# Kernel optimization log

Hardware: AMD Instinct MI355X
Metric: run time of the kernel (lower is better)

## Reference

```python
import jax, jax.numpy as jnp
import numpy as np
from jax import lax

B, S, PH, N = 4, 512, 4096, 16384
D, G, H, L, FF, GS = 1024, 128, 8, 4, 4096, 32
HD = D // H


def setup_inputs() -> dict:
    key = jax.random.key(0)
    ks = list(jax.random.split(key, 16))
    r = lambda k, sh: jax.random.normal(k, sh, jnp.float32) * 0.02
    return {
        'last_hidden': jax.random.normal(ks[0], (B, S, PH), jnp.float32),
        'current_pointcloud': jax.random.normal(ks[1], (B, N, 3), jnp.float32),
        'fp_w': r(ks[2], (D, PH)), 'fp_b': jnp.zeros((D,), jnp.float32),
        'sp_w': r(ks[3], (G * D, D)), 'sp_b': jnp.zeros((G * D,), jnp.float32),
        'pos_embed': r(ks[4], (1, G, D)),
        'ln1_w': jnp.ones((L, D), jnp.float32), 'ln1_b': jnp.zeros((L, D), jnp.float32),
        'in_w': r(ks[5], (L, 3 * D, D)), 'in_b': jnp.zeros((L, 3 * D), jnp.float32),
        'out_w': r(ks[6], (L, D, D)), 'out_b': jnp.zeros((L, D), jnp.float32),
        'ln2_w': jnp.ones((L, D), jnp.float32), 'ln2_b': jnp.zeros((L, D), jnp.float32),
        'mlp_w1': r(ks[7], (L, FF, D)), 'mlp_b1': jnp.zeros((L, FF), jnp.float32),
        'mlp_w2': r(ks[8], (L, D, FF)), 'mlp_b2': jnp.zeros((L, D), jnp.float32),
        'c1_w': r(ks[9], (D, D)), 'c1_b': jnp.zeros((D,), jnp.float32),
        'bn_g': jnp.ones((D,), jnp.float32), 'bn_beta': jnp.zeros((D,), jnp.float32),
        'bn_m': jnp.zeros((D,), jnp.float32), 'bn_v': jnp.ones((D,), jnp.float32),
        'c2_w': r(ks[10], (3 * GS, D)), 'c2_b': jnp.zeros((3 * GS,), jnp.float32),
    }


def _ln(x, w, b):
    m = jnp.mean(x, -1, keepdims=True)
    v = jnp.mean(jnp.square(x - m), -1, keepdims=True)
    return (x - m) * lax.rsqrt(v + 1e-5) * w + b


def _fps(xyz, num_samples):
    # iterative farthest point sampling; deterministic start index 0
    Bb, Nn, _ = xyz.shape
    dist0 = jnp.full((Bb, Nn), 1e10, xyz.dtype)
    far0 = jnp.zeros((Bb,), jnp.int32)

    def step(carry, _):
        dist, far = carry
        centroid = jnp.take_along_axis(xyz, far[:, None, None], axis=1)  # [B,1,3]
        d = jnp.sum(jnp.square(xyz - centroid), -1)                      # [B,N]
        dist = jnp.minimum(dist, d)
        return (dist, jnp.argmax(dist, -1).astype(jnp.int32)), far

    _, cents = lax.scan(step, (dist0, far0), None, length=num_samples)
    cents = cents.T  # [B, num_samples]
    return jnp.take_along_axis(xyz, cents[:, :, None], axis=1)  # [B,num_samples,3]


def reference(last_hidden, current_pointcloud, fp_w, fp_b, sp_w, sp_b, pos_embed,
              ln1_w, ln1_b, in_w, in_b, out_w, out_b, ln2_w, ln2_b,
              mlp_w1, mlp_b1, mlp_w2, mlp_b2,
              c1_w, c1_b, bn_g, bn_beta, bn_m, bn_v, c2_w, c2_b):
    bsz = last_hidden.shape[0]
    agg = jnp.mean(last_hidden @ fp_w.T + fp_b, axis=1)          # [B,D]
    x = (agg @ sp_w.T + sp_b).reshape(bsz, G, D)                 # [B,G,D]
    centers = _fps(current_pointcloud, G)                        # [B,G,3]
    scale = 1.0 / np.sqrt(HD).astype(np.float32)

    def block(x, p):
        l1w, l1b, iw, ib, ow, ob, l2w, l2b, w1, b1, w2, b2 = p
        xn = _ln(x + pos_embed, l1w, l1b)
        qkv = xn @ iw.T + ib                                     # [B,G,3D]
        q, k, v = jnp.split(qkv, 3, axis=-1)
        hsp = lambda t: t.reshape(bsz, G, H, HD).transpose(0, 2, 1, 3)
        q, k, v = hsp(q), hsp(k), hsp(v)
        a = jax.nn.softmax(jnp.einsum('bhqd,bhkd->bhqk', q, k) * scale, axis=-1)
        o = jnp.einsum('bhqk,bhkd->bhqd', a, v).transpose(0, 2, 1, 3).reshape(bsz, G, D)
        x = x + o @ ow.T + ob
        h = jax.nn.gelu(_ln(x, l2w, l2b) @ w1.T + b1, approximate=False)
        return x + h @ w2.T + b2, None

    x, _ = lax.scan(block, x, (ln1_w, ln1_b, in_w, in_b, out_w, out_b,
                               ln2_w, ln2_b, mlp_w1, mlp_b1, mlp_w2, mlp_b2))

    # future_predictor: 1x1 conv == per-token linear; BN in eval mode
    h = x @ c1_w.T + c1_b
    h = jax.nn.relu((h - bn_m) * lax.rsqrt(bn_v + 1e-5) * bn_g + bn_beta)
    deltas = (h @ c2_w.T + c2_b).reshape(bsz * G, GS, 3)
    pred = deltas + centers.reshape(bsz * G, 1, 3)
    return pred.reshape(bsz, G * GS, 3)
```

## Files before the change

### kernel.cpp

```cpp
#include <hip/hip_runtime.h>
#include <hip/hip_bf16.h>
#include <math.h>


typedef __bf16 bf16x8_t __attribute__((ext_vector_type(8)));
typedef float  f32x4_t  __attribute__((ext_vector_type(4)));

__device__ __forceinline__ float wredsum(float v){
#pragma unroll
  for (int o = 32; o; o >>= 1) v += __shfl_down(v, o, 64);
  return v;
}

__device__ __forceinline__ bf16x8_t pack8(float4 a, float4 b){
  bf16x8_t v;
  v[0]=(__bf16)a.x; v[1]=(__bf16)a.y; v[2]=(__bf16)a.z; v[3]=(__bf16)a.w;
  v[4]=(__bf16)b.x; v[5]=(__bf16)b.y; v[6]=(__bf16)b.z; v[7]=(__bf16)b.w;
  return v;
}

__device__ __forceinline__ void gload16(const void* g, void* l){
  __builtin_amdgcn_global_load_lds((const __attribute__((address_space(1))) unsigned int*)g,
                                   (__attribute__((address_space(3))) unsigned int*)l, 16, 0, 0);
}

__global__ __launch_bounds__(1024) void fused_front(
  const float* __restrict__ pc, float* __restrict__ centers,
  const float* __restrict__ agg, const float* __restrict__ spw,
  const float* __restrict__ spb, float* __restrict__ x,
  const float* __restrict__ inw, const float* __restrict__ outw,
  const float* __restrict__ w1, const float* __restrict__ w2,
  const float* __restrict__ c1w, __bf16* __restrict__ wbf)
{
  const int bid = blockIdx.x;
  const int tid = threadIdx.x;
  if (bid < 4){
    const int b = bid;
    const int lane = tid & 63;
    const float* base = pc + (size_t)b * 16384 * 3;
    float px[16], py[16], pz[16], dist[16];
    {
      union { float4 v4[12]; float f[48]; } u;
      const float4* src = (const float4*)(base + tid * 48);
#pragma unroll
      for (int q = 0; q < 12; ++q) u.v4[q] = src[q];
#pragma unroll
      for (int j = 0; j < 16; ++j){
        px[j] = u.f[j*3]; py[j] = u.f[j*3+1]; pz[j] = u.f[j*3+2];
        dist[j] = 1e10f;
      }
    }
    __shared__ unsigned long long keyslot[128];
    for (int i = tid; i < 128; i += 1024) keyslot[i] = 0ULL;
    __syncthreads();
    float cx = base[0], cy = base[1], cz = base[2];
    for (int t = 0; t < 128; ++t){
      if (tid == 0){
        centers[(b*128+t)*3+0] = cx;
        centers[(b*128+t)*3+1] = cy;
        centers[(b*128+t)*3+2] = cz;
      }
      if (t == 127) break;
      float bmax = -1.0f; int bidx = 0;
#pragma unroll
      for (int j = 0; j < 16; ++j){
        float dx = __fsub_rn(px[j], cx);
        float dy = __fsub_rn(py[j], cy);
        float dz = __fsub_rn(pz[j], cz);
        float d  = __fadd_rn(__fadd_rn(__fmul_rn(dx,dx), __fmul_rn(dy,dy)), __fmul_rn(dz,dz));
        float nd = fminf(dist[j], d);
        dist[j] = nd;
        if (nd > bmax){ bmax = nd; bidx = tid*16 + j; }
      }
      unsigned long long key = ((unsigned long long)__float_as_uint(bmax) << 32)
                             | (unsigned long long)(0xFFFFFFFFu - (unsigned)bidx);
#pragma unroll
      for (int o = 32; o; o >>= 1){
        unsigned long long ok = __shfl_down(key, o, 64);
        if (ok > key) key = ok;
      }
      if (lane == 0) atomicMax(&keyslot[t], key);
      __syncthreads();
      const unsigned long long gk = keyslot[t];
      const unsigned gidx = 0xFFFFFFFFu - (unsigned)(gk & 0xFFFFFFFFu);
      const float* cp = base + (size_t)gidx*3;
      cx = cp[0]; cy = cp[1]; cz = cp[2];
    }
  } else if (bid < 1028){
    __shared__ float ag[4096];
    for (int i = tid; i < 4096; i += 1024) ag[i] = agg[i];
    __syncthreads();
    const int wv = tid >> 6, lane = tid & 63;
    const int rbase = ((bid - 4)*16 + wv)*8;
    for (int rr = 0; rr < 8; ++rr){
      const int row = rbase + rr;
      const float* wp = spw + (size_t)row*1024 + lane*4;
      const float4 w0 = *(const float4*)(wp      );
      const float4 wq1 = *(const float4*)(wp + 256);
      const float4 wq2 = *(const float4*)(wp + 512);
      const float4 wq3 = *(const float4*)(wp + 768);
      float acc[4];
#pragma unroll
      for (int bb = 0; bb < 4; ++bb){
        const float* gp = &ag[bb*1024 + lane*4];
        const float4 g0 = *(const float4*)(gp      );
        const float4 g1 = *(const float4*)(gp + 256);
        const float4 g2 = *(const float4*)(gp + 512);
        const float4 g3 = *(const float4*)(gp + 768);
        acc[bb] = w0.x*g0.x + w0.y*g0.y + w0.z*g0.z + w0.w*g0.w
                + wq1.x*g1.x + wq1.y*g1.y + wq1.z*g1.z + wq1.w*g1.w
                + wq2.x*g2.x + wq2.y*g2.y + wq2.z*g2.z + wq2.w*g2.w
                + wq3.x*g3.x + wq3.y*g3.y + wq3.z*g3.z + wq3.w*g3.w;
      }
      float a0 = wredsum(acc[0]);
      float a1 = wredsum(acc[1]);
      float a2 = wredsum(acc[2]);
      float a3 = wredsum(acc[3]);
      if (lane == 0){
        const float bias = spb[row];
        x[(size_t)0*131072 + row] = a0 + bias;
        x[(size_t)1*131072 + row] = a1 + bias;
        x[(size_t)2*131072 + row] = a2 + bias;
        x[(size_t)3*131072 + row] = a3 + bias;
      }
    }
  } else {
    const size_t t = (size_t)(bid - 1028)*1024 + tid;
    const size_t i = t*8;
    const float* src;
    if (i < 50331648){
      const size_t l = i / 12582912, r = i - l*12582912;
      if (r < 3145728)       src = inw  + l*3145728 + r;
      else if (r < 4194304)  src = outw + l*1048576 + (r-3145728);
      else if (r < 8388608)  src = w1   + l*4194304 + (r-4194304);
      else                   src = w2   + l*4194304 + (r-8388608);
    } else src = c1w + (i - 50331648);
    float4 a = *(const float4*)src, bq = *(const float4*)(src+4);
    *(bf16x8_t*)(wbf + i) = pack8(a, bq);
  }
}

__global__ __launch_bounds__(256) void partial_kernel(const float* __restrict__ lh,
                                                      float* __restrict__ part){
  const int ph = blockIdx.x*256 + threadIdx.x;
  const int sc = blockIdx.y, b = blockIdx.z;
  const float* p = lh + ((size_t)b*512 + sc*64)*4096 + ph;
  float s0=0,s1=0,s2=0,s3=0;
  for (int j = 0; j < 64; j += 4){
    s0 += p[(size_t)(j+0)*4096];
    s1 += p[(size_t)(j+1)*4096];
    s2 += p[(size_t)(j+2)*4096];
    s3 += p[(size_t)(j+3)*4096];
  }
  part[(size_t)(b*8+sc)*4096 + ph] = (s0+s1)+(s2+s3);
}

__global__ __launch_bounds__(256) void combine_kernel(const float* __restrict__ part,
                                                      float* __restrict__ mlh){
  const int i = blockIdx.x*256 + threadIdx.x;
  const int b = i >> 12, ph = i & 4095;
  float s = 0;
#pragma unroll
  for (int sc = 0; sc < 8; ++sc) s += part[(size_t)(b*8+sc)*4096 + ph];
  mlh[i] = s * (1.0f/512.0f);
}

__global__ __launch_bounds__(256) void agg_kernel(const float* __restrict__ mlh,
                                                  const float* __restrict__ fpw,
                                                  const float* __restrict__ fpb,
                                                  float* __restrict__ agg){
  const int o = blockIdx.x*4 + (threadIdx.x>>6);
  const int lane = threadIdx.x & 63;
  const int b = o >> 10, d = o & 1023;
  const float* mp = mlh + b*4096;
  const float* wp = fpw + (size_t)d*4096;
  float s = 0;
#pragma unroll 4
  for (int j = 0; j < 64; ++j){
    int ph = lane + j*64;
    s += mp[ph] * wp[ph];
  }
  s = wredsum(s);
  if (lane == 0) agg[o] = s + fpb[d];
}

__global__ __launch_bounds__(256) void ln_kernel(const float* __restrict__ x,
                                                 const float* __restrict__ pos,
                                                 const float* __restrict__ w,
                                                 const float* __restrict__ bb,
                                                 __bf16* __restrict__ out){
  const int tok = blockIdx.x, g = tok & 127, t = threadIdx.x;
  const int lane = t & 63, wv = t >> 6;
  const float* xr = x + (size_t)tok*1024;
  float v[4];
#pragma unroll
  for (int j = 0; j < 4; ++j){
    int d = t + j*256;
    float val = xr[d];
    if (pos) val += pos[g*1024 + d];
    v[j] = val;
  }
  __shared__ float r1[4], r2[4];
  float s = wredsum(v[0]+v[1]+v[2]+v[3]);
  if (lane == 0) r1[wv] = s;
  __syncthreads();
  const float mean = (r1[0]+r1[1]+r1[2]+r1[3]) * (1.0f/1024.0f);
  float sq = 0;
#pragma unroll
  for (int j = 0; j < 4; ++j){ float d0 = v[j]-mean; sq += d0*d0; }
  sq = wredsum(sq);
  if (lane == 0) r2[wv] = sq;
  __syncthreads();
  const float var = (r2[0]+r2[1]+r2[2]+r2[3]) * (1.0f/1024.0f);
  const float rs = rsqrtf(var + 1e-5f);
#pragma unroll
  for (int j = 0; j < 4; ++j){
    int d = t + j*256;
    out[(size_t)tok*1024 + d] = (__bf16)((v[j]-mean)*rs*w[d] + bb[d]);
  }
}

__global__ __launch_bounds__(256) void gemm_sk(
  const __bf16* __restrict__ A, const __bf16* __restrict__ W,
  float* __restrict__ parts, int M, int N, int K, int kc)
{
  __shared__ __bf16 As[4][128*32];
  __shared__ __bf16 Ws[4][128*32];
  const int n0 = blockIdx.x*128, m0 = blockIdx.y*128, z = blockIdx.z;
  const int tid = threadIdx.x;
  const int lane = tid & 63, w = tid >> 6;
  const int wm = w >> 1, wn = w & 1;
  const int lr = lane & 15, g = lane >> 4;
  const int kbeg = z*kc;
  const int nst = kc >> 5;
  const int c0 = tid, c1 = tid + 256;
  const int r0 = c0 >> 2, q0 = c0 & 3;
  const int r1 = c1 >> 2, q1 = c1 & 3;
  const __bf16* a0 = A + (size_t)(m0 + r0)*K + kbeg + q0*8;
  const __bf16* a1 = A + (size_t)(m0 + r1)*K + kbeg + q1*8;
  const __bf16* w0 = W + (size_t)(n0 + r0)*K + kbeg + q0*8;
  const __bf16* w1 = W + (size_t)(n0 + r1)*K + kbeg + q1*8;

#define STAGE(BUF, KOFF) do { \
    gload16(a0 + (KOFF), &As[(BUF)][c0*8]); \
    gload16(a1 + (KOFF), &As[(BUF)][c1*8]); \
    gload16(w0 + (KOFF), &Ws[(BUF)][c0*8]); \
    gload16(w1 + (KOFF), &Ws[(BUF)][c1*8]); \
  } while(0)

  STAGE(0, 0);
  STAGE(1, 32);
  STAGE(2, 64);
  f32x4_t acc[4][4] = {};
  for (int t = 0; t < nst; ++t){
    asm volatile("s_waitcnt vmcnt(8)" ::: "memory");
    __builtin_amdgcn_s_barrier();
    const int tnext = (t+3 < nst) ? (t+3) : (nst-1);
    STAGE((t+3)&3, tnext*32);
    const int cb = t & 3;
    bf16x8_t af[4], bf[4];
#pragma unroll
    for (int f = 0; f < 4; ++f){
      af[f] = *(bf16x8_t*)&As[cb][(wm*64 + f*16 + lr)*32 + g*8];
      bf[f] = *(bf16x8_t*)&Ws[cb][(wn*64 + f*16 + lr)*32 + g*8];
    }
#pragma unroll
    for (int i = 0; i < 4; ++i)
#pragma unroll
      for (int j = 0; j < 4; ++j)
        acc[i][j] = __builtin_amdgcn_mfma_f32_16x16x32_bf16(af[i], bf[j], acc[i][j], 0, 0, 0);
  }
#undef STAGE
  float* C = parts + (size_t)z*M*N;
#pragma unroll
  for (int i = 0; i < 4; ++i)
#pragma unroll
    for (int j = 0; j < 4; ++j)
#pragma unroll
      for (int r = 0; r < 4; ++r){
        const int row = m0 + wm*64 + i*16 + g*4 + r;
        const int col = n0 + wn*64 + j*16 + lr;
        C[(size_t)row*N + col] = acc[i][j][r];
      }
}

__global__ __launch_bounds__(256) void comb_qkv(const float* __restrict__ parts,
                                                const float* __restrict__ bias,
                                                __bf16* __restrict__ out){
  const int i = blockIdx.x*256 + threadIdx.x;
  const int col = i % 3072;
  out[i] = (__bf16)(parts[i] + parts[1572864 + i] + bias[col]);
}

__global__ __launch_bounds__(256) void comb_gelu(const float* __restrict__ parts,
                                                 const float* __restrict__ bias,
                                                 __bf16* __restrict__ out){
  const int i = blockIdx.x*256 + threadIdx.x;
  const int col = i & 4095;
  float v = parts[i] + parts[2097152 + i] + bias[col];
  v = v * 0.5f * (1.0f + erff(v * 0.70710678118654752440f));
  out[i] = (__bf16)v;
}

template<int MODE>
__global__ __launch_bounds__(256) void comb_res_ln(const float* __restrict__ parts, int nsplit,
                                                   const float* __restrict__ bias,
                                                   const float* __restrict__ pos,
                                                   const float* __restrict__ lw,
                                                   const float* __restrict__ lb,
                                                   float* __restrict__ x,
                                                   __bf16* __restrict__ xn){
  const int tok = blockIdx.x, gi = tok & 127, t = threadIdx.x;
  const int lane = t & 63, wv = t >> 6;
  float v[4];
#pragma unroll
  for (int j = 0; j < 4; ++j){
    const int d = t + j*256;
    const size_t idx = (size_t)tok*1024 + d;
    float s = 0;
    for (int z = 0; z < nsplit; ++z) s += parts[(size_t)z*524288 + idx];
    float val = x[idx] + s + bias[d];
    x[idx] = val;
    v[j] = val;
  }
  if (MODE == 2){
#pragma unroll
    for (int j = 0; j < 4; ++j){
      const int d = t + j*256;
      xn[(size_t)tok*1024 + d] = (__bf16)v[j];
    }
    return;
  }
  float u[4];
#pragma unroll
  for (int j = 0; j < 4; ++j){
    const int d = t + j*256;
    u[j] = v[j] + (MODE == 1 ? pos[gi*1024 + d] : 0.0f);
  }
  __shared__ float r1[4], r2[4];
  float s1 = wredsum(u[0]+u[1]+u[2]+u[3]);
  if (lane == 0) r1[wv] = s1;
  __syncthreads();
  const float mean = (r1[0]+r1[1]+r1[2]+r1[3]) * (1.0f/1024.0f);
  float sq = 0;
#pragma unroll
  for (int j = 0; j < 4; ++j){ float d0 = u[j]-mean; sq += d0*d0; }
  sq = wredsum(sq);
  if (lane == 0) r2[wv] = sq;
  __syncthreads();
  const float var = (r2[0]+r2[1]+r2[2]+r2[3]) * (1.0f/1024.0f);
  const float rs = rsqrtf(var + 1e-5f);
#pragma unroll
  for (int j = 0; j < 4; ++j){
    const int d = t + j*256;
    xn[(size_t)tok*1024 + d] = (__bf16)((u[j]-mean)*rs*lw[d] + lb[d]);
  }
}

__global__ __launch_bounds__(256) void attn_fused(const __bf16* __restrict__ qkv,
                                                  __bf16* __restrict__ O){
  const int bh = blockIdx.x >> 1, half = blockIdx.x & 1;
  const int b = bh>>3, h = bh&7;
  const int tid = threadIdx.x, w = tid>>6, lane = tid&63;
  const int lr = lane&15, g = lane>>4;
  __shared__ __bf16 vt[128*128];
  __shared__ __bf16 pl[4*2048];
  {
    const int n = tid >> 1, kh = tid & 1;
    const __bf16* vbase = qkv + (size_t)(b*128)*3072 + 2048 + h*128 + n;
#pragma unroll
    for (int jb = 0; jb < 8; ++jb){
      bf16x8_t pk;
#pragma unroll
      for (int e = 0; e < 8; ++e) pk[e] = vbase[(size_t)(kh*64 + jb*8 + e)*3072];
      const int cb = kh*8 + jb;
      *(bf16x8_t*)&vt[n*128 + ((cb ^ (n&7)) * 8)] = pk;
    }
  }
  const __bf16* qbase = qkv + (size_t)(b*128)*3072 + h*128;
  const __bf16* kbase = qbase + 1024;
  const int qrow0 = half*64 + w*16;
  f32x4_t acc[8] = {};
#pragma unroll
  for (int ks = 0; ks < 4; ++ks){
    bf16x8_t aq, bk[8];
    aq = *(const bf16x8_t*)(qbase + (size_t)(qrow0 + lr)*3072 + ks*32 + g*8);
#pragma unroll
    for (int j = 0; j < 8; ++j)
      bk[j] = *(const bf16x8_t*)(kbase + (size_t)(j*16 + lr)*3072 + ks*32 + g*8);
#pragma unroll
    for (int j = 0; j < 8; ++j)
      acc[j] = __builtin_amdgcn_mfma_f32_16x16x32_bf16(aq, bk[j], acc[j], 0, 0, 0);
  }
  __syncthreads();
  const float scale = 0.088388347648318447f;
#pragma unroll
  for (int r = 0; r < 4; ++r){
    const int row = g*4 + r;
    float sv[8];
    float mx = -1e30f;
#pragma unroll
    for (int j = 0; j < 8; ++j){ sv[j] = acc[j][r]*scale; mx = fmaxf(mx, sv[j]); }
#pragma unroll
    for (int o = 1; o < 16; o <<= 1) mx = fmaxf(mx, __shfl_xor(mx, o, 64));
    float s = 0;
#pragma unroll
    for (int j = 0; j < 8; ++j){ sv[j] = expf(sv[j]-mx); s += sv[j]; }
#pragma unroll
    for (int o = 1; o < 16; o <<= 1) s += __shfl_xor(s, o, 64);
    const float inv = 1.0f/s;
#pragma unroll
    for (int j = 0; j < 8; ++j){
      const int col = j*16 + lr;
      const int slot = (col>>3) ^ (row&7);
      pl[w*2048 + row*128 + slot*8 + (lr&7)] = (__bf16)(sv[j]*inv);
    }
  }
  __syncthreads();
  f32x4_t acc2[8] = {};
#pragma unroll
  for (int ks = 0; ks < 4; ++ks){
    bf16x8_t ap, bv[8];
    {
      const int row = lr;
      const int slot = (ks*4 + g) ^ (row&7);
      ap = *(bf16x8_t*)&pl[w*2048 + row*128 + slot*8];
    }
#pragma unroll
    for (int j = 0; j < 8; ++j){
      const int rowv = j*16 + lr;
      const int cb = ks*4 + g;
      bv[j] = *(bf16x8_t*)&vt[rowv*128 + ((cb ^ (rowv&7))*8)];
    }
#pragma unroll
    for (int j = 0; j < 8; ++j)
      acc2[j] = __builtin_amdgcn_mfma_f32_16x16x32_bf16(ap, bv[j], acc2[j], 0, 0, 0);
  }
#pragma unroll
  for (int j = 0; j < 8; ++j)
#pragma unroll
    for (int r = 0; r < 4; ++r){
      const int row = qrow0 + g*4 + r;
      const int col = j*16 + lr;
      O[(size_t)(b*128+row)*1024 + h*128 + col] = (__bf16)acc2[j][r];
    }
}

__global__ __launch_bounds__(256) void head_kernel(const float* __restrict__ parts,
                                                   const float* __restrict__ c1b,
                                                   const float* __restrict__ bnm,
                                                   const float* __restrict__ bnv,
                                                   const float* __restrict__ bng,
                                                   const float* __restrict__ bnb,
                                                   const float* __restrict__ c2w,
                                                   const float* __restrict__ c2b,
                                                   const float* __restrict__ centers,
                                                   float* __restrict__ out){
  const int tok = blockIdx.x, t = threadIdx.x;
  const int wv = t >> 6, lane = t & 63;
  __shared__ float hrow[1024];
#pragma unroll
  for (int j = 0; j < 4; ++j){
    const int d = t + j*256;
    const size_t idx = (size_t)tok*1024 + d;
    float s = 0;
#pragma unroll
    for (int z = 0; z < 8; ++z) s += parts[(size_t)z*524288 + idx];
    float v = s + c1b[d];
    v = (v - bnm[d]) * rsqrtf(bnv[d] + 1e-5f) * bng[d] + bnb[d];
    hrow[d] = fmaxf(v, 0.0f);
  }
  __syncthreads();
  for (int i = 0; i < 24; ++i){
    const int n = wv*24 + i;
    const float* wp = c2w + (size_t)n*1024;
    float s = 0;
#pragma unroll 4
    for (int j = 0; j < 16; ++j){
      const int k = lane + j*64;
      s += hrow[k] * wp[k];
    }
    s = wredsum(s);
    if (lane == 0) out[(size_t)tok*96 + n] = s + c2b[n] + centers[tok*3 + (n % 3)];
  }
}

extern "C" void kernel_launch(void* const* d_in, const int* in_sizes, int n_in,
                              void* d_out, int out_size, void* d_ws, size_t ws_size,
                              hipStream_t stream){
  const float* lh   = (const float*)d_in[0];
  const float* pc   = (const float*)d_in[1];
  const float* fpw  = (const float*)d_in[2];
  const float* fpb  = (const float*)d_in[3];
  const float* spw  = (const float*)d_in[4];
  const float* spb  = (const float*)d_in[5];
  const float* pos  = (const float*)d_in[6];
  const float* ln1w = (const float*)d_in[7];
  const float* ln1b = (const float*)d_in[8];
  const float* inw  = (const float*)d_in[9];
  const float* inb  = (const float*)d_in[10];
  const float* outw = (const float*)d_in[11];
  const float* outb = (const float*)d_in[12];
  const float* ln2w = (const float*)d_in[13];
  const float* ln2b = (const float*)d_in[14];
  const float* w1   = (const float*)d_in[15];
  const float* b1   = (const float*)d_in[16];
  const float* w2   = (const float*)d_in[17];
  const float* b2   = (const float*)d_in[18];
  const float* c1w  = (const float*)d_in[19];
  const float* c1b  = (const float*)d_in[20];
  const float* bng  = (const float*)d_in[21];
  const float* bnbt = (const float*)d_in[22];
  const float* bnm  = (const float*)d_in[23];
  const float* bnv  = (const float*)d_in[24];
  const float* c2w  = (const float*)d_in[25];
  const float* c2b  = (const float*)d_in[26];
  float* out = (float*)d_out;

  float* f = (float*)d_ws;
  float* parts = f;              f += 16*524288;
  float* part  = f;              f += 131072;
  float* mlh   = f;              f += 16384;
  float* agg   = f;              f += 4096;
  float* x     = f;              f += 524288;
  float* cent  = f;              f += 2048;
  __bf16* bfp = (__bf16*)f;
  __bf16* xn   = bfp;            bfp += 524288;
  __bf16* qkv  = bfp;            bfp += 1572864;
  __bf16* obuf = bfp;            bfp += 524288;
  __bf16* hbf  = bfp;            bfp += 2097152;
  __bf16* xbf  = bfp;            bfp += 524288;
  __bf16* wbf  = bfp;            bfp += 51380224;

  partial_kernel<<<dim3(16,8,4), 256, 0, stream>>>(lh, part);
  combine_kernel<<<64, 256, 0, stream>>>(part, mlh);
  agg_kernel<<<1024, 256, 0, stream>>>(mlh, fpw, fpb, agg);
  fused_front<<<7300, 1024, 0, stream>>>(pc, cent, agg, spw, spb, x,
                                         inw, outw, w1, w2, c1w, wbf);
  ln_kernel<<<512, 256, 0, stream>>>(x, pos, ln1w, ln1b, xn);

  for (int l = 0; l < 4; ++l){
    const __bf16* wl = wbf + (size_t)l*12582912;
    gemm_sk<<<dim3(24,4,2), 256, 0, stream>>>(xn, wl, parts, 512, 3072, 1024, 512);
    comb_qkv<<<6144, 256, 0, stream>>>(parts, inb + l*3072, qkv);
    attn_fused<<<64, 256, 0, stream>>>(qkv, obuf);
    gemm_sk<<<dim3(8,4,8), 256, 0, stream>>>(obuf, wl + 3145728, parts, 512, 1024, 1024, 128);
    comb_res_ln<0><<<512, 256, 0, stream>>>(parts, 8, outb + l*1024, nullptr,
                                            ln2w + l*1024, ln2b + l*1024, x, xn);
    gemm_sk<<<dim3(32,4,2), 256, 0, stream>>>(xn, wl + 4194304, parts, 512, 4096, 1024, 512);
    comb_gelu<<<8192, 256, 0, stream>>>(parts, b1 + l*4096, hbf);
    gemm_sk<<<dim3(8,4,8), 256, 0, stream>>>(hbf, wl + 8388608, parts, 512, 1024, 4096, 512);
    if (l < 3)
      comb_res_ln<1><<<512, 256, 0, stream>>>(parts, 8, b2 + l*1024, pos,
                                              ln1w + (l+1)*1024, ln1b + (l+1)*1024, x, xn);
    else
      comb_res_ln<2><<<512, 256, 0, stream>>>(parts, 8, b2 + l*1024, nullptr,
                                              nullptr, nullptr, x, xbf);
  }

  gemm_sk<<<dim3(8,4,8), 256, 0, stream>>>(xbf, wbf + 50331648, parts, 512, 1024, 1024, 128);
  head_kernel<<<512, 256, 0, stream>>>(parts, c1b, bnm, bnv, bng, bnbt, c2w, c2b, cent, out);
}
```

Measured before the change: 825.4 us.

## Use single-buffered BK=64 tiles with XOR-swizzled LDS in split-K GEMM

Replaces the 4-stage BK=32 pipelined LDS ring in the split-K GEMM with a single 128x64 tile per operand, loaded and consumed between two barriers. The global-to-LDS addresses are XOR-swizzled by row so the MFMA fragment reads avoid LDS bank conflicts. This halves the number of barrier iterations and removes bank conflicts, but gives up overlapping global loads with MFMA compute, so memory latency is now exposed every iteration.

```diff
diff --git a/kernel.cpp b/kernel.cpp
--- a/kernel.cpp
+++ b/kernel.cpp
@@ -224,53 +224,56 @@
   const __bf16* __restrict__ A, const __bf16* __restrict__ W,
   float* __restrict__ parts, int M, int N, int K, int kc)
 {
-  __shared__ __bf16 As[4][128*32];
-  __shared__ __bf16 Ws[4][128*32];
+  __shared__ __bf16 As[128*64];
+  __shared__ __bf16 Ws[128*64];
   const int n0 = blockIdx.x*128, m0 = blockIdx.y*128, z = blockIdx.z;
   const int tid = threadIdx.x;
   const int lane = tid & 63, w = tid >> 6;
   const int wm = w >> 1, wn = w & 1;
   const int lr = lane & 15, g = lane >> 4;
-  const int kbeg = z*kc;
-  const int nst = kc >> 5;
-  const int c0 = tid, c1 = tid + 256;
-  const int r0 = c0 >> 2, q0 = c0 & 3;
-  const int r1 = c1 >> 2, q1 = c1 & 3;
-  const __bf16* a0 = A + (size_t)(m0 + r0)*K + kbeg + q0*8;
-  const __bf16* a1 = A + (size_t)(m0 + r1)*K + kbeg + q1*8;
-  const __bf16* w0 = W + (size_t)(n0 + r0)*K + kbeg + q0*8;
-  const __bf16* w1 = W + (size_t)(n0 + r1)*K + kbeg + q1*8;
-
-#define STAGE(BUF, KOFF) do { \
-    gload16(a0 + (KOFF), &As[(BUF)][c0*8]); \
-    gload16(a1 + (KOFF), &As[(BUF)][c1*8]); \
-    gload16(w0 + (KOFF), &Ws[(BUF)][c0*8]); \
-    gload16(w1 + (KOFF), &Ws[(BUF)][c1*8]); \
-  } while(0)
-
-  STAGE(0, 0);
-  STAGE(1, 32);
-  STAGE(2, 64);
+  const int kbeg = z*kc, kend = kbeg + kc;
+  const int c0 = tid, c1 = tid+256, c2 = tid+512, c3 = tid+768;
+  const int r0 = c0>>3, r1 = c1>>3, r2 = c2>>3, r3 = c3>>3;
+  const int s0 = ((c0&7) ^ (r0&7))*8, s1 = ((c1&7) ^ (r1&7))*8;
+  const int s2 = ((c2&7) ^ (r2&7))*8, s3 = ((c3&7) ^ (r3&7))*8;
+  const __bf16* pa0 = A + (size_t)(m0+r0)*K + kbeg + s0;
+  const __bf16* pa1 = A + (size_t)(m0+r1)*K + kbeg + s1;
+  const __bf16* pa2 = A + (size_t)(m0+r2)*K + kbeg + s2;
+  const __bf16* pa3 = A + (size_t)(m0+r3)*K + kbeg + s3;
+  const __bf16* pw0 = W + (size_t)(n0+r0)*K + kbeg + s0;
+  const __bf16* pw1 = W + (size_t)(n0+r1)*K + kbeg + s1;
+  const __bf16* pw2 = W + (size_t)(n0+r2)*K + kbeg + s2;
+  const __bf16* pw3 = W + (size_t)(n0+r3)*K + kbeg + s3;
   f32x4_t acc[4][4] = {};
-  for (int t = 0; t < nst; ++t){
-    asm volatile("s_waitcnt vmcnt(8)" ::: "memory");
-    __builtin_amdgcn_s_barrier();
-    const int tnext = (t+3 < nst) ? (t+3) : (nst-1);
-    STAGE((t+3)&3, tnext*32);
-    const int cb = t & 3;
-    bf16x8_t af[4], bf[4];
-#pragma unroll
-    for (int f = 0; f < 4; ++f){
-      af[f] = *(bf16x8_t*)&As[cb][(wm*64 + f*16 + lr)*32 + g*8];
-      bf[f] = *(bf16x8_t*)&Ws[cb][(wn*64 + f*16 + lr)*32 + g*8];
-    }
-#pragma unroll
-    for (int i = 0; i < 4; ++i)
-#pragma unroll
-      for (int j = 0; j < 4; ++j)
-        acc[i][j] = __builtin_amdgcn_mfma_f32_16x16x32_bf16(af[i], bf[j], acc[i][j], 0, 0, 0);
-  }
-#undef STAGE
+  for (int k0 = 0; k0 < kc; k0 += 64){
+    __syncthreads();
+    gload16(pa0 + k0, &As[c0*8]);
+    gload16(pa1 + k0, &As[c1*8]);
+    gload16(pa2 + k0, &As[c2*8]);
+    gload16(pa3 + k0, &As[c3*8]);
+    gload16(pw0 + k0, &Ws[c0*8]);
+    gload16(pw1 + k0, &Ws[c1*8]);
+    gload16(pw2 + k0, &Ws[c2*8]);
+    gload16(pw3 + k0, &Ws[c3*8]);
+    __syncthreads();
+#pragma unroll
+    for (int ks2 = 0; ks2 < 2; ++ks2){
+      bf16x8_t af[4], bf[4];
+#pragma unroll
+      for (int f = 0; f < 4; ++f){
+        const int ra = wm*64 + f*16 + lr;
+        const int rb = wn*64 + f*16 + lr;
+        const int lq = ks2*4 + g;
+        af[f] = *(bf16x8_t*)&As[ra*64 + (lq ^ (ra&7))*8];
+        bf[f] = *(bf16x8_t*)&Ws[rb*64 + (lq ^ (rb&7))*8];
+      }
+#pragma unroll
+      for (int i = 0; i < 4; ++i)
+#pragma unroll
+        for (int j = 0; j < 4; ++j)
+          acc[i][j] = __builtin_amdgcn_mfma_f32_16x16x32_bf16(af[i], bf[j], acc[i][j], 0, 0, 0);
+    }
+  }
   float* C = parts + (size_t)z*M*N;
 #pragma unroll
   for (int i = 0; i < 4; ++i)
```

Result: faster. 798.7 us (-3.2%).
